# Performance work log

Hardware: AMD Instinct MI355X
Metric: run time of the kernel (lower is better)

## Reference

```python
import jax, jax.numpy as jnp
import numpy as np
from jax import lax

D = 256      # key/query dim
D_F = 256    # diff feature channels
C_TOK = 1    # leading context tokens in query_vit
EPS = 1e-6


def conv2d(x, w, b, pad):
    out = lax.conv_general_dilated(x, w, (1, 1), [(pad, pad), (pad, pad)],
                                   dimension_numbers=('NCHW', 'OIHW', 'NCHW'))
    return out + b[None, :, None, None]


def gn1(x, g, b):
    # GroupNorm with 1 group: normalize over (C,H,W) per sample
    mu = jnp.mean(x, axis=(1, 2, 3), keepdims=True)
    var = jnp.var(x, axis=(1, 2, 3), keepdims=True)
    xn = (x - mu) * lax.rsqrt(var + EPS)
    return xn * g[None, :, None, None] + b[None, :, None, None]


def resize_bilinear_ac(x, Ho, Wo):
    # F.interpolate(mode='bilinear', align_corners=True)
    B, C, H, W = x.shape
    ys = jnp.linspace(0.0, H - 1.0, Ho)
    xs = jnp.linspace(0.0, W - 1.0, Wo)
    y0 = jnp.floor(ys).astype(jnp.int32)
    y1 = jnp.minimum(y0 + 1, H - 1)
    wy = (ys - y0)[None, None, :, None]
    x0 = jnp.floor(xs).astype(jnp.int32)
    x1 = jnp.minimum(x0 + 1, W - 1)
    wx = (xs - x0)[None, None, None, :]
    r = x[:, :, y0, :] * (1.0 - wy) + x[:, :, y1, :] * wy
    return r[:, :, :, x0] * (1.0 - wx) + r[:, :, :, x1] * wx


def setup_inputs() -> dict:
    key = jax.random.key(0)
    ks = jax.random.split(key, 12)
    B, Hd, Wd, Ht, Wt = 8, 64, 64, 32, 32

    def kaiming(k, shape, fan_in):
        return jax.random.normal(k, shape, jnp.float32) * np.sqrt(2.0 / fan_in)

    return {
        'query_vit': jax.random.normal(ks[0], (B, C_TOK + Ht * Wt, D), jnp.float32),
        'feat_diff_cat': jax.random.normal(ks[1], (B, 5 * D_F, Hd, Wd), jnp.float32),
        'rb_w1': kaiming(ks[2], (D_F, 5 * D_F, 3, 3), 5 * D_F * 9), 'rb_b1': jnp.zeros((D_F,), jnp.float32),
        'rb_w2': kaiming(ks[3], (D_F, D_F, 3, 3), D_F * 9), 'rb_b2': jnp.zeros((D_F,), jnp.float32),
        'rb_ws': kaiming(ks[4], (D_F, 5 * D_F, 1, 1), 5 * D_F), 'rb_bs': jnp.zeros((D_F,), jnp.float32),
        'ln_g': jnp.ones((D_F,), jnp.float32), 'ln_b': jnp.zeros((D_F,), jnp.float32),
        'key_w': kaiming(ks[5], (D, D_F, 1, 1), D_F), 'key_b': jnp.zeros((D,), jnp.float32),
        'val_w': kaiming(ks[6], (D_F, D_F, 1, 1), D_F), 'val_b': jnp.zeros((D_F,), jnp.float32),
        'dh0_w': kaiming(ks[7], (D_F, D_F, 3, 3), D_F * 9), 'dh0_b': jnp.zeros((D_F,), jnp.float32),
        'dh1_w': kaiming(ks[8], (D_F, D_F, 3, 3), D_F * 9), 'dh1_b': jnp.zeros((D_F,), jnp.float32),
    }


def reference(query_vit, feat_diff_cat, rb_w1, rb_b1, rb_w2, rb_b2, rb_ws, rb_bs,
              ln_g, ln_b, key_w, key_b, val_w, val_b, dh0_w, dh0_b, dh1_w, dh1_b):
    B, _, h_diff, w_diff = feat_diff_cat.shape
    N = query_vit.shape[1] - C_TOK
    h_trm = w_trm = int(N ** 0.5)

    # ResBlock_ysh(D_f*5 -> D_f): conv3x3 + relu + conv3x3, 1x1-projected residual
    h = jax.nn.relu(conv2d(feat_diff_cat, rb_w1, rb_b1, 1))
    h = conv2d(h, rb_w2, rb_b2, 1)
    feat_diff = jax.nn.relu(h + conv2d(feat_diff_cat, rb_ws, rb_bs, 0))

    fln = gn1(feat_diff, ln_g, ln_b)
    key_diff = conv2d(fln, key_w, key_b, 0).reshape(B, D, -1)          # (B, D, HW)
    value_diff = conv2d(fln, val_w, val_b, 0).reshape(B, D_F, -1)      # (B, Df, HW)
    value_diff = jnp.transpose(value_diff, (0, 2, 1))                  # (B, HW, Df)

    # cross attention: (B, C+N, D) @ (B, D, HW) -> softmax -> @ (B, HW, Df)
    scores = jnp.einsum('bnd,bdm->bnm', query_vit, key_diff) * (D ** -0.5)
    attn = jax.nn.softmax(scores, axis=-1)
    out_cross = jnp.einsum('bnm,bmf->bnf', attn, value_diff)           # (B, C+N, Df)

    out_cross_c = out_cross[:, :C_TOK, :]
    out_p = jnp.transpose(out_cross[:, C_TOK:, :], (0, 2, 1)).reshape(B, D_F, h_trm, w_trm)
    out_p = jax.nn.relu(conv2d(out_p, dh0_w, dh0_b, 1))
    out_p = resize_bilinear_ac(out_p, h_diff, w_diff)
    out_p = out_p + feat_diff                                          # DropPath(0) = identity
    out_p = jax.nn.relu(conv2d(gn1(out_p, ln_g, ln_b), dh1_w, dh1_b, 1)) + out_p
    return out_cross_c, out_p
```

## Files before the change

### kernel.cpp

```cpp
#include <hip/hip_runtime.h>
#include <cstdint>
#include <cstddef>

typedef __attribute__((ext_vector_type(4))) float     f32x4;
typedef __attribute__((ext_vector_type(8))) __bf16    bf16x8;
typedef __attribute__((ext_vector_type(8))) short     short8;
typedef __attribute__((ext_vector_type(4))) unsigned short u16x4;
typedef unsigned short u16;

__device__ __forceinline__ float b2f(u16 u) {
  unsigned x = ((unsigned)u) << 16;
  float f;
  __builtin_memcpy(&f, &x, 4);
  return f;
}
__device__ __forceinline__ u16 f2b(float f) {
  unsigned u;
  __builtin_memcpy(&u, &f, 4);
  return (u16)((u + 0x7FFFu + ((u >> 16) & 1u)) >> 16);
}

struct GP {
  const u16*  A;
  const u16*  B;
  const float* bias;
  const void* aux;
  void*       C;
  float*      out0;
  float*      st;
  long long   aBS, bBS, cBS, auxBS, biasBS;
  int Ktot, Mrows, ldc;
  int cin, logW, wpad, poff;
  float scale;
};

#define GLDS16(g, l)                                                        \
  __builtin_amdgcn_global_load_lds(                                         \
      (const void __attribute__((address_space(1)))*)(g),                   \
      (void __attribute__((address_space(3)))*)(l), 16, 0, 0)

struct G256 {
  const u16* A;
  const u16* B;
  float* P;
  long long aBS;
  int Ktot, cin, logW, wpad, poff;
};

__global__ __launch_bounds__(512, 2) void k_gemm256(G256 gp) {
  const int tid = threadIdx.x;
  const int l = tid & 63, w = tid >> 6;
  const int lr = l & 15, lc = l >> 4;
  const int id = blockIdx.x;
  const int xcd = id & 7, slot = id >> 3;
  const int sp = xcd >> 2;
  const int u = (xcd & 3) * 32 + slot;
  const int mt = u & 15;
  const int b = u >> 4;
  const int m0 = mt << 8;
  const int wm = w >> 2, wn = w & 3;

  __shared__ __align__(16) u16 sm[4][16384];
  u16* smb = &sm[0][0];

  f32x4 acc[8][4];
#pragma unroll
  for (int i = 0; i < 8; ++i)
#pragma unroll
    for (int j = 0; j < 4; ++j) acc[i][j] = (f32x4){0.f, 0.f, 0.f, 0.f};

  const u16* Ab = gp.A + (size_t)b * gp.aBS;
  const u16* aS[2];
  const u16* bS[2];
#pragma unroll
  for (int j = 0; j < 2; ++j) {
    const int r = j * 128 + w * 16 + (l >> 2);
    const int p = m0 + r;
    const int y = p >> gp.logW, x = p & ((1 << gp.logW) - 1);
    const int sw = ((l & 3) ^ ((r >> 1) & 3)) << 3;
    aS[j] = Ab + (size_t)((y + gp.poff) * gp.wpad + (x + gp.poff)) * gp.cin + sw;
    bS[j] = gp.B + (size_t)r * gp.Ktot + sw;
  }

  const int NH = gp.Ktot >> 6;
  const int kt0h = sp * NH;
  int off = kt0h << 5;
  int tap = off / gp.cin;
  int kcS = off - tap * gp.cin;
  int dxS = tap % 3;
  int tapS = (tap / 3) * gp.wpad + dxS;
  int hgS = kt0h;

  auto stage = [&](int h) {
    const int hb = h & 3;
    const int kB = hgS << 5;
    const int kA = tapS * gp.cin + kcS;
    kcS += 32;
    if (kcS == gp.cin) {
      kcS = 0; ++dxS; ++tapS;
      if (dxS == 3) { dxS = 0; tapS += gp.wpad - 3; }
    }
    ++hgS;
    u16* base = smb + hb * 16384 + (w * 16) * 32 + l * 8;
    GLDS16(aS[0] + kA, base);
    GLDS16(aS[1] + kA, base + 4096);
    GLDS16(bS[0] + kB, base + 8192);
    GLDS16(bS[1] + kB, base + 12288);
  };

  stage(0);
  stage(1);
  stage(2);
  asm volatile("s_waitcnt vmcnt(8)" ::: "memory");
  __builtin_amdgcn_s_barrier();

  bf16x8 av[8], bv[4];
  {
    const char* b0 = (const char*)smb;
#pragma unroll
    for (int mi = 0; mi < 8; ++mi) {
      const int row = wm * 128 + mi * 16 + lr;
      av[mi] = *(const bf16x8*)(b0 + row * 64 + ((lc ^ ((row >> 1) & 3)) << 4));
    }
#pragma unroll
    for (int ni = 0; ni < 4; ++ni) {
      const int row = wn * 64 + ni * 16 + lr;
      bv[ni] = *(const bf16x8*)(b0 + 16384 + row * 64 +
                                ((lc ^ ((row >> 1) & 3)) << 4));
    }
  }

  for (int h = 0; h < NH; ++h) {
    if (h + 3 < NH) stage(h + 3);
    const int rem = NH - 1 - h;
    if (rem > 0) {
      if (rem > 2)
        asm volatile("s_waitcnt vmcnt(8)" ::: "memory");
      else if (rem == 2)
        asm volatile("s_waitcnt vmcnt(4)" ::: "memory");
      else
        asm volatile("s_waitcnt vmcnt(0)" ::: "memory");
      asm volatile("s_waitcnt lgkmcnt(0)" ::: "memory");
      __builtin_amdgcn_s_barrier();
    }

    const bool pf = (h + 1 < NH);
    const char* nxt = (const char*)smb + ((h + 1) & 3) * 32768;

#pragma unroll
    for (int mi = 0; mi < 8; ++mi) {
      const int row = wm * 128 + mi * 16 + lr;
      const int sw = (lc ^ ((row >> 1) & 3)) << 4;
#pragma unroll
      for (int ni = 0; ni < 4; ++ni)
        acc[mi][ni] = __builtin_amdgcn_mfma_f32_16x16x32_bf16(
            av[mi], bv[ni], acc[mi][ni], 0, 0, 0);
      if (pf) av[mi] = *(const bf16x8*)(nxt + row * 64 + sw);
    }
    if (pf) {
#pragma unroll
      for (int ni = 0; ni < 4; ++ni) {
        const int row = wn * 64 + ni * 16 + lr;
        bv[ni] = *(const bf16x8*)(nxt + 16384 + row * 64 +
                                  ((lc ^ ((row >> 1) & 3)) << 4));
      }
    }
  }

  float* P = gp.P + ((size_t)sp * 128 + b * 16 + mt) * 65536;
#pragma unroll
  for (int mi = 0; mi < 8; ++mi)
#pragma unroll
    for (int ni = 0; ni < 4; ++ni) {
      const int ncol = wn * 64 + ni * 16 + lr;
      const int mloc = wm * 128 + mi * 16 + lc * 4;
#pragma unroll
      for (int r = 0; r < 4; ++r)
        P[(size_t)(mloc + r) * 256 + ncol] = acc[mi][ni][r];
    }
}

__global__ __launch_bounds__(256) void k_reduceH1(const float* __restrict__ P,
                                                  const float* __restrict__ bias,
                                                  u16* __restrict__ o) {
  const int i4 = blockIdx.x * 256 + threadIdx.x;
  const int flat = i4 << 2;
  const int n0 = flat & 255;
  const int mloc = (flat >> 8) & 255;
  const int gm = flat >> 16;
  const f32x4 a = *(const f32x4*)(P + (size_t)gm * 65536 + mloc * 256 + n0);
  const f32x4 c = *(const f32x4*)(P + (size_t)(128 + gm) * 65536 + mloc * 256 + n0);
  const f32x4 bb = *(const f32x4*)(bias + n0);
  const int batch = gm >> 4;
  const int mg = (gm & 15) * 256 + mloc;
  const int y = mg >> 6, x = mg & 63;
  u16x4 r;
#pragma unroll
  for (int k = 0; k < 4; ++k) r[k] = f2b(fmaxf(a[k] + c[k] + bb[k], 0.f));
  *(u16x4*)(o + ((size_t)batch * 4356 + (size_t)(y + 1) * 66 + x + 1) * 256 + n0) = r;
}

template <int AMODE, int CW>
__global__ __launch_bounds__(512, 2) void k_gemm8(GP gp) {
  const int tid = threadIdx.x;
  const int l = tid & 63, w = tid >> 6;
  const int b = blockIdx.z;
  const int m0 = blockIdx.x * 128;
  const int wm = w >> 2, wn = w & 3;
  const int lr = l & 15, lc = l >> 4;

  __shared__ __align__(16) u16 sm[2][24576];

  f32x4 acc[4][4];
#pragma unroll
  for (int i = 0; i < 4; ++i)
#pragma unroll
    for (int j = 0; j < 4; ++j) acc[i][j] = (f32x4){0.f, 0.f, 0.f, 0.f};

  const u16* Ab = gp.A + (size_t)b * gp.aBS;
  const u16* Bb = gp.B + (size_t)b * gp.bBS;
  const int scoff = (((tid & 7) ^ ((tid >> 3) & 7)) << 3);

  const u16* aP[2];
  const u16* aP2[2];
#pragma unroll
  for (int i = 0; i < 2; ++i) {
    const int p = m0 + i * 64 + (tid >> 3);
    const int y = p >> 6, x = p & 63;
    aP[i] = Ab + (size_t)(y * 66 + x) * gp.cin + scoff;
    if (AMODE == 2) {
      const u16* Xb = (const u16*)gp.aux + (size_t)b * gp.auxBS;
      aP2[i] = Xb + (size_t)((y + 1) * 66 + (x + 1)) * 1280 + scoff;
    }
  }
  const u16* bP[4];
#pragma unroll
  for (int i = 0; i < 4; ++i)
    bP[i] = Bb + (size_t)(i * 64 + (tid >> 3)) * gp.Ktot + scoff;

  const int NT = gp.Ktot >> 6;
  const int seg1t = (AMODE == 2) ? 36 : 0x7fffffff;
  int kcS = 0, tapS = 0, dxS = 0, nstg = 0;

  auto stage = [&](int buf) {
    const int kt = nstg++;
    const int kB = kt << 6;
    u16* sA = &sm[buf][0] + (w << 9);
    u16* sB = &sm[buf][8192] + (w << 9);
    if (AMODE == 2 && kt >= seg1t) {
      const int kA = (kt - seg1t) << 6;
      GLDS16(aP2[0] + kA, sA);
      GLDS16(aP2[1] + kA, sA + 4096);
    } else {
      const int kA = tapS * gp.cin + kcS;
      kcS += 64;
      if (kcS == gp.cin) {
        kcS = 0; ++dxS; ++tapS;
        if (dxS == 3) { dxS = 0; tapS += 63; }
      }
      GLDS16(aP[0] + kA, sA);
      GLDS16(aP[1] + kA, sA + 4096);
    }
    GLDS16(bP[0] + kB, sB);
    GLDS16(bP[1] + kB, sB + 4096);
    GLDS16(bP[2] + kB, sB + 8192);
    GLDS16(bP[3] + kB, sB + 12288);
  };

  stage(0);
  asm volatile("s_waitcnt vmcnt(0)" ::: "memory");
  __builtin_amdgcn_s_barrier();

  for (int t = 0; t < NT; ++t) {
    const int buf = t & 1;
    const u16* sAc = &sm[buf][0];
    const u16* sBc = &sm[buf][8192];
    if (t + 1 < NT) stage(buf ^ 1);

    bf16x8 av0[4], av1[4], bv0[4], bv1[4];
#pragma unroll
    for (int mi = 0; mi < 4; ++mi) {
      const int row = wm * 64 + mi * 16 + lr;
      av0[mi] = *(const bf16x8*)(sAc + row * 64 + (((0 + lc) ^ (row & 7)) << 3));
      av1[mi] = *(const bf16x8*)(sAc + row * 64 + (((4 + lc) ^ (row & 7)) << 3));
    }
#pragma unroll
    for (int ni = 0; ni < 4; ++ni) {
      const int row = wn * 64 + ni * 16 + lr;
      bv0[ni] = *(const bf16x8*)(sBc + row * 64 + (((0 + lc) ^ (row & 7)) << 3));
      bv1[ni] = *(const bf16x8*)(sBc + row * 64 + (((4 + lc) ^ (row & 7)) << 3));
    }
#pragma unroll
    for (int mi = 0; mi < 4; ++mi)
#pragma unroll
      for (int ni = 0; ni < 4; ++ni)
        acc[mi][ni] = __builtin_amdgcn_mfma_f32_16x16x32_bf16(
            av0[mi], bv0[ni], acc[mi][ni], 0, 0, 0);
#pragma unroll
    for (int mi = 0; mi < 4; ++mi)
#pragma unroll
      for (int ni = 0; ni < 4; ++ni)
        acc[mi][ni] = __builtin_amdgcn_mfma_f32_16x16x32_bf16(
            av1[mi], bv1[ni], acc[mi][ni], 0, 0, 0);
    asm volatile("s_waitcnt vmcnt(0)" ::: "memory");
    __builtin_amdgcn_s_barrier();
  }

  float lsum = 0.f, lsq = 0.f;
#pragma unroll
  for (int mi = 0; mi < 4; ++mi) {
#pragma unroll
    for (int ni = 0; ni < 4; ++ni) {
      const int ncol = wn * 64 + ni * 16 + lr;
      const int mbase = m0 + wm * 64 + mi * 16 + lc * 4;
      const float bv_ = gp.bias[ncol];
      if constexpr (CW == 8) {
        float* F = (float*)gp.C + (size_t)b * gp.cBS;
        u16* FB = (u16*)gp.out0 + (size_t)b * gp.cBS;
#pragma unroll
        for (int r = 0; r < 4; ++r) {
          float v = fmaxf(acc[mi][ni][r] + bv_, 0.f);
          const size_t idx = (size_t)(mbase + r) * 256 + ncol;
          F[idx] = v;
          FB[idx] = f2b(v);
          lsum += v;
          lsq += v * v;
        }
      } else {
        float* Cf =
            (float*)gp.C + (size_t)b * gp.cBS + (size_t)ncol * 4096 + mbase;
        const float* mid = (const float*)gp.aux + (size_t)b * gp.auxBS;
        f32x4 o;
#pragma unroll
        for (int r = 0; r < 4; ++r) {
          float v = fmaxf(acc[mi][ni][r] + bv_, 0.f);
          o[r] = v + mid[(size_t)(mbase + r) * 256 + ncol];
        }
        *(f32x4*)Cf = o;
      }
    }
  }
  if constexpr (CW == 8) {
    __syncthreads();
#pragma unroll
    for (int o = 32; o; o >>= 1) {
      lsum += __shfl_down(lsum, o);
      lsq += __shfl_down(lsq, o);
    }
    float* red = (float*)&sm[0][0];
    if (l == 0) { red[w * 2] = lsum; red[w * 2 + 1] = lsq; }
    __syncthreads();
    if (tid == 0) {
      float s = 0.f, s2 = 0.f;
#pragma unroll
      for (int k = 0; k < 8; ++k) { s += red[k * 2]; s2 += red[k * 2 + 1]; }
      atomicAdd(&gp.st[b * 2], s);
      atomicAdd(&gp.st[b * 2 + 1], s2);
    }
  }
}

template <int AMODE, int CW, bool RELU>
__global__ __launch_bounds__(256, 2) void k_gemm(GP gp) {
  const int tid = threadIdx.x;
  const int l = tid & 63, w = tid >> 6;
  const int b = blockIdx.z;
  const int m0 = blockIdx.x * 128, n0 = blockIdx.y * 128;
  const int wm = w >> 1, wn = w & 1;

  __shared__ __align__(16) u16 smA[128 * 64];
  __shared__ __align__(16) u16 smB[128 * 64];

  f32x4 acc[4][4];
#pragma unroll
  for (int i = 0; i < 4; ++i)
#pragma unroll
    for (int j = 0; j < 4; ++j) acc[i][j] = (f32x4){0.f, 0.f, 0.f, 0.f};

  const u16* Ab = gp.A + (size_t)b * gp.aBS;
  const u16* Bb = gp.B + (size_t)b * gp.bBS;

  const int scoff = (((l & 7) ^ (l >> 3)) << 3);

  const u16* aRow[4];
  const u16* bRow[4];
  u16* ldsA[4];
  u16* ldsB[4];
#pragma unroll
  for (int i = 0; i < 4; ++i) {
    const int r = w * 32 + i * 8 + (l >> 3);
    bRow[i] = Bb + (size_t)(n0 + r) * gp.Ktot + scoff;
    const int p = m0 + r;
    if (AMODE == 0) {
      const int pc = p < gp.Mrows ? p : gp.Mrows - 1;
      aRow[i] = Ab + (size_t)pc * gp.Ktot + scoff;
    } else {
      const int y = p >> gp.logW, x = p & ((1 << gp.logW) - 1);
      const int icoord = (y + gp.poff) * gp.wpad + (x + gp.poff);
      aRow[i] = Ab + (size_t)icoord * gp.cin + scoff;
    }
    ldsA[i] = smA + (w * 32 + i * 8) * 64;
    ldsB[i] = smB + (w * 32 + i * 8) * 64;
  }

  const int ktiles = gp.Ktot >> 6;
  int tap_off = 0, dx = 0, kc = 0;

  for (int kt = 0; kt < ktiles; ++kt) {
    int koffA;
    if (AMODE == 0)
      koffA = kt << 6;
    else
      koffA = tap_off * gp.cin + kc;
    const int koffB = kt << 6;
#pragma unroll
    for (int i = 0; i < 4; ++i) GLDS16(aRow[i] + koffA, ldsA[i]);
#pragma unroll
    for (int i = 0; i < 4; ++i) GLDS16(bRow[i] + koffB, ldsB[i]);

    if (AMODE == 1) {
      kc += 64;
      if (kc == gp.cin) {
        kc = 0;
        ++dx;
        ++tap_off;
        if (dx == 3) { dx = 0; tap_off += gp.wpad - 3; }
      }
    }

    __syncthreads();
#pragma unroll
    for (int ks = 0; ks < 2; ++ks) {
      bf16x8 av[4], bv[4];
      const int cc = (ks << 2) + (l >> 4);
#pragma unroll
      for (int mi = 0; mi < 4; ++mi) {
        const int row = wm * 64 + mi * 16 + (l & 15);
        av[mi] = *(const bf16x8*)((const char*)smA + (row << 7) +
                                  ((cc ^ (row & 7)) << 4));
      }
#pragma unroll
      for (int ni = 0; ni < 4; ++ni) {
        const int row = wn * 64 + ni * 16 + (l & 15);
        bv[ni] = *(const bf16x8*)((const char*)smB + (row << 7) +
                                  ((cc ^ (row & 7)) << 4));
      }
#pragma unroll
      for (int mi = 0; mi < 4; ++mi)
#pragma unroll
        for (int ni = 0; ni < 4; ++ni)
          acc[mi][ni] = __builtin_amdgcn_mfma_f32_16x16x32_bf16(
              av[mi], bv[ni], acc[mi][ni], 0, 0, 0);
    }
    __syncthreads();
  }

#pragma unroll
  for (int mi = 0; mi < 4; ++mi) {
#pragma unroll
    for (int ni = 0; ni < 4; ++ni) {
      const int ncol = n0 + wn * 64 + ni * 16 + (l & 15);
      const int mbase = m0 + wm * 64 + mi * 16 + ((l >> 4) << 2);
      const float bv_ =
          gp.bias ? gp.bias[(size_t)b * gp.biasBS + ncol] : 0.f;

      if constexpr (CW == 7) {
        u16* base = (u16*)gp.C;
        if (ncol < 256) {
#pragma unroll
          for (int r = 0; r < 4; ++r)
            base[(size_t)b * 1048576 + (size_t)(mbase + r) * 256 + ncol] =
                f2b(acc[mi][ni][r] + bv_);
        } else {
          u16x4 pk;
#pragma unroll
          for (int r = 0; r < 4; ++r) pk[r] = f2b(acc[mi][ni][r] + bv_);
          *(u16x4*)(base + 8388608 + (size_t)b * 1048576 +
                    (size_t)(ncol - 256) * 4096 + mbase) = pk;
        }
      } else {
#pragma unroll
        for (int reg = 0; reg < 4; ++reg) {
          const int mrow = mbase + reg;
          if (mrow >= gp.Mrows) continue;
          float v = acc[mi][ni][reg] * gp.scale + bv_;
          if (RELU) v = v > 0.f ? v : 0.f;
          if constexpr (CW == 0) {
            ((u16*)gp.C)[(size_t)b * gp.cBS + (size_t)mrow * gp.ldc + ncol] =
                f2b(v);
          } else if constexpr (CW == 5) {
            ((float*)gp.C)[(size_t)b * gp.cBS + (size_t)mrow * 256 + ncol] = v;
          }
        }
      }
    }
  }
}

__global__ __launch_bounds__(256, 2) void k_attnv(const u16* __restrict__ S,
                                                  const u16* __restrict__ Vv,
                                                  float* __restrict__ PAV) {
  const int tid = threadIdx.x;
  const int l = tid & 63, w = tid >> 6;
  const int b = blockIdx.z >> 2, sp = blockIdx.z & 3;
  const int m0 = blockIdx.x * 128, n0 = blockIdx.y * 128;
  const int wm = w >> 1, wn = w & 1;

  __shared__ __align__(16) u16 smA[128 * 64];
  __shared__ __align__(16) u16 smB[128 * 64];

  f32x4 acc[4][4];
#pragma unroll
  for (int i = 0; i < 4; ++i)
#pragma unroll
    for (int j = 0; j < 4; ++j) acc[i][j] = (f32x4){0.f, 0.f, 0.f, 0.f};

  const u16* Ab = S + (size_t)b * 4198400 + sp * 1024;
  const u16* Bb = Vv + (size_t)b * 1048576 + sp * 1024;
  const int scoff = (((l & 7) ^ (l >> 3)) << 3);

  const u16* aRow[4];
  const u16* bRow[4];
  u16* ldsA[4];
  u16* ldsB[4];
#pragma unroll
  for (int i = 0; i < 4; ++i) {
    const int r = w * 32 + i * 8 + (l >> 3);
    bRow[i] = Bb + (size_t)(n0 + r) * 4096 + scoff;
    const int p = m0 + r;
    const int pc = p < 1025 ? p : 1024;
    aRow[i] = Ab + (size_t)pc * 4096 + scoff;
    ldsA[i] = smA + (w * 32 + i * 8) * 64;
    ldsB[i] = smB + (w * 32 + i * 8) * 64;
  }

  for (int kt = 0; kt < 16; ++kt) {
    const int koff = kt << 6;
#pragma unroll
    for (int i = 0; i < 4; ++i) GLDS16(aRow[i] + koff, ldsA[i]);
#pragma unroll
    for (int i = 0; i < 4; ++i) GLDS16(bRow[i] + koff, ldsB[i]);

    __syncthreads();
#pragma unroll
    for (int ks = 0; ks < 2; ++ks) {
      bf16x8 av[4], bv[4];
      const int cc = (ks << 2) + (l >> 4);
#pragma unroll
      for (int mi = 0; mi < 4; ++mi) {
        const int row = wm * 64 + mi * 16 + (l & 15);
        av[mi] = *(const bf16x8*)((const char*)smA + (row << 7) +
                                  ((cc ^ (row & 7)) << 4));
      }
#pragma unroll
      for (int ni = 0; ni < 4; ++ni) {
        const int row = wn * 64 + ni * 16 + (l & 15);
        bv[ni] = *(const bf16x8*)((const char*)smB + (row << 7) +
                                  ((cc ^ (row & 7)) << 4));
      }
#pragma unroll
      for (int mi = 0; mi < 4; ++mi)
#pragma unroll
        for (int ni = 0; ni < 4; ++ni)
          acc[mi][ni] = __builtin_amdgcn_mfma_f32_16x16x32_bf16(
              av[mi], bv[ni], acc[mi][ni], 0, 0, 0);
    }
    __syncthreads();
  }

  float* P = PAV + (size_t)blockIdx.z * 262400;
#pragma unroll
  for (int mi = 0; mi < 4; ++mi) {
#pragma unroll
    for (int ni = 0; ni < 4; ++ni) {
      const int ncol = n0 + wn * 64 + ni * 16 + (l & 15);
      const int mbase = m0 + wm * 64 + mi * 16 + ((l >> 4) << 2);
#pragma unroll
      for (int r = 0; r < 4; ++r) {
        const int mrow = mbase + r;
        if (mrow >= 1025) continue;
        P[(size_t)mrow * 256 + ncol] = acc[mi][ni][r];
      }
    }
  }
}

__global__ __launch_bounds__(256) void k_reduceAttn(const float* __restrict__ PAV,
                                                    float* __restrict__ out0,
                                                    u16* __restrict__ OCP) {
  const int b = blockIdx.y;
  const int i4 = blockIdx.x * 256 + threadIdx.x;
  if (i4 >= 65600) return;
  const int flat = i4 << 2;
  const int row = flat >> 8;
  const int col = flat & 255;
  const float* base = PAV + (size_t)(b * 4) * 262400 + (size_t)row * 256 + col;
  f32x4 s = *(const f32x4*)base;
  s += *(const f32x4*)(base + 262400);
  s += *(const f32x4*)(base + 524800);
  s += *(const f32x4*)(base + 787200);
  if (row == 0) {
    *(f32x4*)(out0 + (size_t)b * 256 + col) = s;
  } else {
    const int p = row - 1, y = p >> 5, x = p & 31;
    u16x4 r;
#pragma unroll
    for (int k = 0; k < 4; ++k) r[k] = f2b(s[k]);
    *(u16x4*)(OCP + ((size_t)b * 1156 + (size_t)(y + 1) * 34 + x + 1) * 256 +
              col) = r;
  }
}


__global__ __launch_bounds__(256) void k_prep_x(const float* __restrict__ x,
                                                u16* __restrict__ o) {
  __shared__ float t[32][65];
  const int b = blockIdx.z, c0 = blockIdx.y << 5, y = blockIdx.x;
  const float* src = x + ((size_t)b * 1280 + c0) * 4096 + (size_t)y * 64;
#pragma unroll
  for (int i = 0; i < 8; ++i) {
    const int idx = threadIdx.x + (i << 8);
    const int c = idx >> 6, xx = idx & 63;
    t[c][xx] = src[(size_t)c * 4096 + xx];
  }
  __syncthreads();
  u16* dst = o + ((size_t)b * 4356 + (size_t)(y + 1) * 66 + 1) * 1280 + c0;
  const int xx = threadIdx.x >> 2;
  const int cq = (threadIdx.x & 3) << 3;
  short8 pk;
#pragma unroll
  for (int j = 0; j < 8; ++j) pk[j] = (short)f2b(t[cq + j][xx]);
  *(short8*)(dst + (size_t)xx * 1280 + cq) = pk;
}

__device__ __forceinline__ void zb1(u16* p, int P, int C, int idx) {
  const int per_img = (4 * P - 4) * C;
  const int b = idx / per_img;
  const int r = idx % per_img;
  const int pix = r / C, c = r % C;
  int y, x;
  const int Pm = P - 1;
  if (pix < P) { y = 0; x = pix; }
  else if (pix < 2 * P) { y = Pm; x = pix - P; }
  else if (pix < 3 * P - 2) { y = pix - 2 * P + 1; x = 0; }
  else { y = pix - (3 * P - 2) + 1; x = Pm; }
  p[((size_t)b * P * P + (size_t)y * P + x) * C + c] = 0;
}

__global__ __launch_bounds__(256) void k_zero_borders(u16* XPAD, u16* H1,
                                                      u16* G2, u16* OCP) {
  const int nx = 8 * 260 * 1280;
  const int nh = 8 * 260 * 256;
  const int no = 8 * 132 * 256;
  const int total = nx + 2 * nh + no;
  for (int i = blockIdx.x * 256 + threadIdx.x; i < total;
       i += gridDim.x * 256) {
    if (i < nx) zb1(XPAD, 66, 1280, i);
    else if (i < nx + nh) zb1(H1, 66, 256, i - nx);
    else if (i < nx + 2 * nh) zb1(G2, 66, 256, i - nx - nh);
    else zb1(OCP, 34, 256, i - nx - 2 * nh);
  }
}

__global__ __launch_bounds__(256) void k_prep_all(
    const float* __restrict__ w1, const float* __restrict__ w2,
    const float* __restrict__ wsc, const float* __restrict__ wd0,
    const float* __restrict__ wd1, const float* __restrict__ b2,
    const float* __restrict__ bsc, const float* __restrict__ q,
    u16* __restrict__ W1R, u16* __restrict__ WCAT2, u16* __restrict__ WD0R,
    u16* __restrict__ WD1R, float* __restrict__ BB2, u16* __restrict__ QB) {
  const int N1 = 2949120, N2 = 917504, N3 = 589824, N4 = 589824,
            N5 = 2099200, N6 = 256;
  const int T = N1 + N2 + N3 + N4 + N5 + N6;
  for (int i = blockIdx.x * 256 + threadIdx.x; i < T; i += gridDim.x * 256) {
    if (i < N1) {
      const int ci = i % 1280, r = i / 1280, t = r % 9, co = r / 9;
      W1R[i] = f2b(w1[((size_t)co * 1280 + ci) * 9 + t]);
    } else if (i < N1 + N2) {
      const int k = i - N1;
      const int co = k / 3584, kk = k % 3584;
      float v;
      if (kk < 2304) {
        const int tap = kk / 256, ci = kk % 256;
        v = w2[((size_t)co * 256 + ci) * 9 + tap];
      } else {
        v = wsc[(size_t)co * 1280 + (kk - 2304)];
      }
      WCAT2[k] = f2b(v);
    } else if (i < N1 + N2 + N3) {
      const int k = i - N1 - N2;
      const int ci = k % 256, r = k / 256, t = r % 9, co = r / 9;
      WD0R[k] = f2b(wd0[((size_t)co * 256 + ci) * 9 + t]);
    } else if (i < N1 + N2 + N3 + N4) {
      const int k = i - N1 - N2 - N3;
      const int ci = k % 256, r = k / 256, t = r % 9, co = r / 9;
      WD1R[k] = f2b(wd1[((size_t)co * 256 + ci) * 9 + t]);
    } else if (i < N1 + N2 + N3 + N4 + N5) {
      const int k = i - N1 - N2 - N3 - N4;
      QB[k] = f2b(q[k] * 0.0625f);
    } else {
      const int k = i - N1 - N2 - N3 - N4 - N5;
      BB2[k] = b2[k] + bsc[k];
    }
  }
}

__global__ __launch_bounds__(256) void k_foldkv(
    const float* __restrict__ wk, const float* __restrict__ wv,
    const float* __restrict__ bk, const float* __restrict__ bv,
    const float* __restrict__ g, const float* __restrict__ lnb,
    const float* __restrict__ st, u16* __restrict__ WKVB,
    float* __restrict__ BKVB) {
  const int idx = blockIdx.x * 256 + threadIdx.x;
  const int b = idx >> 9, j = idx & 511;
  const float mu = st[b * 2] * (1.f / 1048576.f);
  const float var = st[b * 2 + 1] * (1.f / 1048576.f) - mu * mu;
  const float rs = rsqrtf(var + 1e-6f);
  const float* wrow = (j < 256) ? wk + (size_t)j * 256 : wv + (size_t)(j - 256) * 256;
  float acc = (j < 256) ? bk[j] : bv[j - 256];
  u16* orow = WKVB + ((size_t)b * 512 + j) * 256;
  for (int c = 0; c < 256; ++c) {
    const float wv_ = wrow[c];
    orow[c] = f2b(wv_ * g[c] * rs);
    acc += wv_ * (lnb[c] - mu * rs * g[c]);
  }
  BKVB[b * 512 + j] = acc;
}

template <bool PAD>
__global__ __launch_bounds__(256) void k_gn_norm(const float* __restrict__ x,
                                                 const float* __restrict__ st,
                                                 const float* __restrict__ g,
                                                 const float* __restrict__ bb,
                                                 u16* __restrict__ o) {
  const int b = blockIdx.y;
  const float mu = st[b * 2] * (1.f / 1048576.f);
  const float var = st[b * 2 + 1] * (1.f / 1048576.f) - mu * mu;
  const float rs = rsqrtf(var + 1e-6f);
  const int i4 = blockIdx.x * 256 + threadIdx.x;
  const f32x4 v = ((const f32x4*)(x + (size_t)b * 1048576))[i4];
  const int flat = i4 << 2;
  const int c = flat & 255;
  const int p = flat >> 8;
  const f32x4 gv = *(const f32x4*)(g + c);
  const f32x4 bv = *(const f32x4*)(bb + c);
  u16x4 r;
#pragma unroll
  for (int k = 0; k < 4; ++k) r[k] = f2b((v[k] - mu) * rs * gv[k] + bv[k]);
  size_t oidx;
  if (PAD) {
    const int y = p >> 6, xx = p & 63;
    oidx = ((size_t)b * 4356 + (size_t)(y + 1) * 66 + xx + 1) * 256 + c;
  } else {
    oidx = ((size_t)b * 4096 + p) * 256 + c;
  }
  *(u16x4*)(o + oidx) = r;
}

__global__ __launch_bounds__(256) void k_softmax(u16* __restrict__ s) {
  const size_t row = blockIdx.x;
  u16* p = s + row * 4096;
  const int t = threadIdx.x;
  const short8 r0 = ((const short8*)p)[t];
  const short8 r1 = ((const short8*)p)[t + 256];
  float v[16];
#pragma unroll
  for (int i = 0; i < 8; ++i) {
    v[i] = b2f((u16)r0[i]);
    v[8 + i] = b2f((u16)r1[i]);
  }
  float m = v[0];
#pragma unroll
  for (int i = 1; i < 16; ++i) m = fmaxf(m, v[i]);
#pragma unroll
  for (int o = 32; o; o >>= 1) m = fmaxf(m, __shfl_xor(m, o));
  __shared__ float lm[4], lsum[4];
  const int w = t >> 6;
  if ((t & 63) == 0) lm[w] = m;
  __syncthreads();
  m = fmaxf(fmaxf(lm[0], lm[1]), fmaxf(lm[2], lm[3]));
  float sum = 0.f;
#pragma unroll
  for (int i = 0; i < 16; ++i) {
    v[i] = __expf(v[i] - m);
    sum += v[i];
  }
#pragma unroll
  for (int o = 32; o; o >>= 1) sum += __shfl_xor(sum, o);
  if ((t & 63) == 0) lsum[w] = sum;
  __syncthreads();
  sum = lsum[0] + lsum[1] + lsum[2] + lsum[3];
  const float inv = 1.f / sum;
  short8 o0, o1;
#pragma unroll
  for (int i = 0; i < 8; ++i) {
    o0[i] = (short)f2b(v[i] * inv);
    o1[i] = (short)f2b(v[8 + i] * inv);
  }
  ((short8*)p)[t] = o0;
  ((short8*)p)[t + 256] = o1;
}

__global__ __launch_bounds__(256) void k_resize_add(const float* __restrict__ d0,
                                                    const float* __restrict__ F,
                                                    float* __restrict__ mid,
                                                    float* __restrict__ st) {
  const int b = blockIdx.y;
  const float* db = d0 + (size_t)b * 262144;
  const float* Fb = F + (size_t)b * 1048576;
  float* mb = mid + (size_t)b * 1048576;
  float ls = 0.f, lq = 0.f;
  for (int i4 = blockIdx.x * 256 + threadIdx.x; i4 < 262144;
       i4 += 64 * 256) {
    const int flat = i4 << 2;
    const int c = flat & 255;
    const int p = flat >> 8;
    const int y = p >> 6, x = p & 63;
    const float fy = y * (31.f / 63.f);
    const int y0 = (int)fy;
    const float wy = fy - y0;
    const int y1 = y0 + 1 > 31 ? 31 : y0 + 1;
    const float fx = x * (31.f / 63.f);
    const int x0 = (int)fx;
    const float wx = fx - x0;
    const int x1 = x0 + 1 > 31 ? 31 : x0 + 1;
    const f32x4 a = *(const f32x4*)(db + ((size_t)(y0 * 32 + x0) << 8) + c);
    const f32x4 bq = *(const f32x4*)(db + ((size_t)(y0 * 32 + x1) << 8) + c);
    const f32x4 cq = *(const f32x4*)(db + ((size_t)(y1 * 32 + x0) << 8) + c);
    const f32x4 dq = *(const f32x4*)(db + ((size_t)(y1 * 32 + x1) << 8) + c);
    f32x4 r = (a * (1.f - wx) + bq * wx) * (1.f - wy) +
              (cq * (1.f - wx) + dq * wx) * wy;
    r += *(const f32x4*)(Fb + flat);
    *(f32x4*)(mb + flat) = r;
    ls += r[0] + r[1] + r[2] + r[3];
    lq += r[0] * r[0] + r[1] * r[1] + r[2] * r[2] + r[3] * r[3];
  }
#pragma unroll
  for (int o = 32; o; o >>= 1) {
    ls += __shfl_down(ls, o);
    lq += __shfl_down(lq, o);
  }
  __shared__ float red[8];
  const int w = threadIdx.x >> 6;
  if ((threadIdx.x & 63) == 0) { red[w * 2] = ls; red[w * 2 + 1] = lq; }
  __syncthreads();
  if (threadIdx.x == 0) {
    atomicAdd(&st[16 + b * 2], red[0] + red[2] + red[4] + red[6]);
    atomicAdd(&st[16 + b * 2 + 1], red[1] + red[3] + red[5] + red[7]);
  }
}


extern "C" void kernel_launch(void* const* d_in, const int* in_sizes, int n_in,
                              void* d_out, int out_size, void* d_ws,
                              size_t ws_size, hipStream_t stream) {
  (void)in_sizes; (void)n_in; (void)out_size;

  const float* q   = (const float*)d_in[0];
  const float* xdc = (const float*)d_in[1];
  const float* w1  = (const float*)d_in[2];
  const float* b1  = (const float*)d_in[3];
  const float* w2  = (const float*)d_in[4];
  const float* b2  = (const float*)d_in[5];
  const float* wsc = (const float*)d_in[6];
  const float* bsc = (const float*)d_in[7];
  const float* lng = (const float*)d_in[8];
  const float* lnb = (const float*)d_in[9];
  const float* wk  = (const float*)d_in[10];
  const float* bk  = (const float*)d_in[11];
  const float* wv  = (const float*)d_in[12];
  const float* bv  = (const float*)d_in[13];
  const float* wd0 = (const float*)d_in[14];
  const float* bd0 = (const float*)d_in[15];
  const float* wd1 = (const float*)d_in[16];
  const float* bd1 = (const float*)d_in[17];

  char* ws = (char*)d_ws;
  size_t cur = 0;
  auto alloc = [&](size_t sz) {
    char* p = ws + cur;
    cur += sz;
    return p;
  };
  u16* XPAD  = (u16*)alloc(89194496);
  u16* W1R   = (u16*)alloc(5898240);
  u16* WCAT2 = (u16*)alloc(1835008);
  u16* WD0R  = (u16*)alloc(1179648);
  u16* WD1R  = (u16*)alloc(1179648);
  u16* WKVB  = (u16*)alloc(2097152);
  float* BKVB = (float*)alloc(16384);
  float* BB2 = (float*)alloc(1024);
  u16* H1    = (u16*)alloc(17842176);
  float* F   = (float*)alloc(33554432);
  u16* FB    = (u16*)alloc(16777216);
  u16* KT    = (u16*)alloc(16777216);
  u16* V     = (u16*)alloc(16777216);
  u16* QB    = (u16*)alloc(4198400);
  u16* OCP   = (u16*)alloc(4734976);
  float* D0O = (float*)alloc(8388608);
  float* MID = (float*)alloc(33554432);
  u16* G2    = (u16*)alloc(17842176);
  float* ST  = (float*)alloc(256);
  u16* SCORES = XPAD;
  float* PART = (float*)F;
  float* PAV  = D0O;
  (void)V;

  if (ws_size < cur) return;

  float* out0 = (float*)d_out;
  float* out1 = (float*)d_out + 2048;

  hipMemsetAsync(ST, 0, 256, stream);
  k_zero_borders<<<2048, 256, 0, stream>>>(XPAD, H1, G2, OCP);
  k_prep_x<<<dim3(64, 40, 8), 256, 0, stream>>>(xdc, XPAD);
  k_prep_all<<<4096, 256, 0, stream>>>(w1, w2, wsc, wd0, wd1, b2, bsc, q, W1R,
                                       WCAT2, WD0R, WD1R, BB2, QB);

  {
    G256 g{};
    g.A = XPAD; g.B = W1R; g.P = PART;
    g.aBS = 5575680; g.Ktot = 11520;
    g.cin = 1280; g.logW = 6; g.wpad = 66; g.poff = 0;
    k_gemm256<<<256, 512, 0, stream>>>(g);
    k_reduceH1<<<8192, 256, 0, stream>>>(PART, b1, H1);
  }
  {
    GP g{};
    g.A = H1; g.B = WCAT2; g.bias = BB2; g.aux = XPAD; g.C = F;
    g.out0 = (float*)FB; g.st = ST;
    g.aBS = 1115136; g.bBS = 0; g.cBS = 1048576; g.auxBS = 5575680;
    g.Ktot = 3584; g.Mrows = 4096; g.ldc = 256;
    g.cin = 256; g.logW = 6; g.wpad = 66; g.poff = 0; g.scale = 1.f;
    k_gemm8<2, 8><<<dim3(32, 1, 8), 512, 0, stream>>>(g);
  }
  k_foldkv<<<16, 256, 0, stream>>>(wk, wv, bk, bv, lng, lnb, ST, WKVB, BKVB);
  {
    GP g{};
    g.A = FB; g.B = WKVB; g.bias = BKVB; g.C = KT;
    g.aBS = 1048576; g.bBS = 131072; g.cBS = 0; g.biasBS = 512;
    g.Ktot = 256; g.Mrows = 4096; g.ldc = 256; g.scale = 1.f;
    k_gemm<0, 7, false><<<dim3(32, 4, 8), 256, 0, stream>>>(g);
  }
  {
    GP g{};
    g.A = QB; g.B = KT; g.bias = nullptr; g.C = SCORES;
    g.aBS = 262400; g.bBS = 1048576; g.cBS = 4198400;
    g.Ktot = 256; g.Mrows = 1025; g.ldc = 4096; g.scale = 1.f;
    k_gemm<0, 0, false><<<dim3(9, 32, 8), 256, 0, stream>>>(g);
  }
  k_softmax<<<8200, 256, 0, stream>>>(SCORES);
  k_attnv<<<dim3(9, 2, 32), 256, 0, stream>>>(SCORES, V, PAV);
  k_reduceAttn<<<dim3(257, 8), 256, 0, stream>>>(PAV, out0, OCP);
  {
    GP g{};
    g.A = OCP; g.B = WD0R; g.bias = bd0; g.C = D0O;
    g.aBS = 295936; g.bBS = 0; g.cBS = 262144; g.biasBS = 0;
    g.Ktot = 2304; g.Mrows = 1024; g.ldc = 256;
    g.cin = 256; g.logW = 5; g.wpad = 34; g.poff = 0; g.scale = 1.f;
    k_gemm<1, 5, true><<<dim3(8, 2, 8), 256, 0, stream>>>(g);
  }
  k_resize_add<<<dim3(64, 8), 256, 0, stream>>>(D0O, F, MID, ST);
  k_gn_norm<true><<<dim3(1024, 8), 256, 0, stream>>>(MID, ST + 16, lng, lnb, G2);
  {
    GP g{};
    g.A = G2; g.B = WD1R; g.bias = bd1; g.C = out1; g.aux = MID;
    g.aBS = 1115136; g.bBS = 0; g.cBS = 1048576; g.auxBS = 1048576;
    g.Ktot = 2304; g.Mrows = 4096; g.ldc = 256;
    g.cin = 256; g.logW = 6; g.wpad = 66; g.poff = 0; g.scale = 1.f;
    k_gemm8<1, 6><<<dim3(32, 1, 8), 512, 0, stream>>>(g);
  }
}
```

Before: 661.8 us.

## Prefetch next tile's LDS fragments into registers during MFMA and stage two ahead

Restructures the bf16 MFMA GEMM main loop into a deeper software pipeline. Two K-tiles are staged into shared memory up front, and each iteration issues the global load for tile t+2 into the buffer just consumed. The LDS-to-register loads for tile t+1 are interleaved between the MFMA groups of tile t, so LDS read latency is hidden behind matrix math instead of stalling at the start of each iteration. The cost is a second set of fragment registers kept live across the loop, which can raise register pressure and lower occupancy.

```diff
diff --git a/kernel.cpp b/kernel.cpp
--- a/kernel.cpp
+++ b/kernel.cpp
@@ -268,16 +268,14 @@
   };
 
   stage(0);
+  stage(1);
   asm volatile("s_waitcnt vmcnt(0)" ::: "memory");
   __builtin_amdgcn_s_barrier();
 
-  for (int t = 0; t < NT; ++t) {
-    const int buf = t & 1;
-    const u16* sAc = &sm[buf][0];
-    const u16* sBc = &sm[buf][8192];
-    if (t + 1 < NT) stage(buf ^ 1);
-
-    bf16x8 av0[4], av1[4], bv0[4], bv1[4];
+  bf16x8 av0[4], av1[4], bv0[4], bv1[4];
+  {
+    const u16* sAc = &sm[0][0];
+    const u16* sBc = &sm[0][8192];
 #pragma unroll
     for (int mi = 0; mi < 4; ++mi) {
       const int row = wm * 64 + mi * 16 + lr;
@@ -290,20 +288,55 @@
       bv0[ni] = *(const bf16x8*)(sBc + row * 64 + (((0 + lc) ^ (row & 7)) << 3));
       bv1[ni] = *(const bf16x8*)(sBc + row * 64 + (((4 + lc) ^ (row & 7)) << 3));
     }
-#pragma unroll
-    for (int mi = 0; mi < 4; ++mi)
+  }
+  asm volatile("s_waitcnt lgkmcnt(0)" ::: "memory");
+  __builtin_amdgcn_s_barrier();
+
+  for (int t = 0; t < NT; ++t) {
+    if (t + 2 < NT) stage(t & 1);
+    const bool pf = (t + 1 < NT);
+    const u16* nA = &sm[(t + 1) & 1][0];
+    const u16* nB = &sm[(t + 1) & 1][8192];
+
+#pragma unroll
+    for (int mi = 0; mi < 4; ++mi) {
+      const int row = wm * 64 + mi * 16 + lr;
 #pragma unroll
       for (int ni = 0; ni < 4; ++ni)
         acc[mi][ni] = __builtin_amdgcn_mfma_f32_16x16x32_bf16(
             av0[mi], bv0[ni], acc[mi][ni], 0, 0, 0);
-#pragma unroll
-    for (int mi = 0; mi < 4; ++mi)
+      if (pf)
+        av0[mi] = *(const bf16x8*)(nA + row * 64 + (((0 + lc) ^ (row & 7)) << 3));
+    }
+    if (pf) {
+#pragma unroll
+      for (int ni = 0; ni < 4; ++ni) {
+        const int row = wn * 64 + ni * 16 + lr;
+        bv0[ni] = *(const bf16x8*)(nB + row * 64 + (((0 + lc) ^ (row & 7)) << 3));
+      }
+    }
+#pragma unroll
+    for (int mi = 0; mi < 4; ++mi) {
+      const int row = wm * 64 + mi * 16 + lr;
 #pragma unroll
       for (int ni = 0; ni < 4; ++ni)
         acc[mi][ni] = __builtin_amdgcn_mfma_f32_16x16x32_bf16(
             av1[mi], bv1[ni], acc[mi][ni], 0, 0, 0);
-    asm volatile("s_waitcnt vmcnt(0)" ::: "memory");
-    __builtin_amdgcn_s_barrier();
+      if (pf)
+        av1[mi] = *(const bf16x8*)(nA + row * 64 + (((4 + lc) ^ (row & 7)) << 3));
+    }
+    if (pf) {
+#pragma unroll
+      for (int ni = 0; ni < 4; ++ni) {
+        const int row = wn * 64 + ni * 16 + lr;
+        bv1[ni] = *(const bf16x8*)(nB + row * 64 + (((4 + lc) ^ (row & 7)) << 3));
+      }
+    }
+    if (pf) {
+      asm volatile("s_waitcnt vmcnt(0)" ::: "memory");
+      asm volatile("s_waitcnt lgkmcnt(0)" ::: "memory");
+      __builtin_amdgcn_s_barrier();
+    }
   }
 
   float lsum = 0.f, lsq = 0.f;
```

New measurement: 668.8 us. About the same (+1.1%).
